# Performance work log

Hardware: AMD Instinct MI355X
Metric: run time of the kernel (lower is better)

Reference implementation:

```python
import jax, jax.numpy as jnp
import numpy as np

B, T, D, N, K, H = 2, 2048, 2560, 8, 4, 256
G = N // K
WINDOW = 1024
ROPE_BASE = 10000
K_MASK = -2.3819763e+38
EPS = 1e-6


def apply_rope(inputs, positions, base_frequency):
    # inputs: [B, L, n, H]; positions: [B, L]
    head_dim = inputs.shape[-1]
    fraction = 2 * jnp.arange(0, head_dim // 2) / head_dim
    timescale = base_frequency ** fraction
    sinusoid = positions[..., None] / timescale[None, None, :]   # [B, L, H/2]
    sinusoid = sinusoid[..., None, :]                            # [B, L, 1, H/2]
    sin, cos = jnp.sin(sinusoid), jnp.cos(sinusoid)
    first, second = jnp.split(inputs, 2, axis=-1)
    out = jnp.concatenate([first * cos - second * sin,
                           second * cos + first * sin], axis=-1)
    return out.astype(inputs.dtype)


def rms_norm(x, scale):
    # Gemma-style RMSNorm: normalize over last dim, (1 + scale) gain.
    var = jnp.mean(jnp.square(x), axis=-1, keepdims=True)
    return x * jax.lax.rsqrt(var + EPS) * (1.0 + scale)


def setup_inputs() -> dict:
    key = jax.random.key(0)
    ks = jax.random.split(key, 5)
    x = jax.random.normal(ks[0], (B, T, D), jnp.float32)
    positions = jnp.broadcast_to(jnp.arange(T, dtype=jnp.int32), (B, T))
    # Causal sliding-window mask (LOCAL_SLIDING, window=1024), shape [B, 1, T, S].
    qp = jnp.arange(T)[:, None]
    kp = jnp.arange(T)[None, :]
    mask = (kp <= qp) & ((qp - kp) < WINDOW)
    attn_mask = jnp.broadcast_to(mask[None, None], (B, 1, T, T))
    q_w = jax.random.normal(ks[1], (N, D, H), jnp.float32) * 0.02
    kv_w = jax.random.normal(ks[2], (2, K, D, H), jnp.float32) * 0.02
    q_scale = jnp.zeros((H,), jnp.float32)
    k_scale = jnp.zeros((H,), jnp.float32)
    out_w = jax.random.normal(ks[3], (N, H, D), jnp.float32) * 0.02
    return {"x": x, "q_w": q_w, "kv_w": kv_w, "q_scale": q_scale,
            "k_scale": k_scale, "out_w": out_w,
            "positions": positions, "attn_mask": attn_mask}


def reference(x, q_w, kv_w, q_scale, k_scale, out_w, positions, attn_mask):
    dtype = x.dtype
    # GQA projections (num_kv_heads != num_heads branch)
    q = jnp.einsum('BTD,NDH->BTNH', x, q_w)          # [B,T,N,H]
    k = jnp.einsum('BSD,KDH->BSKH', x, kv_w[0])      # [B,S,K,H]
    v = jnp.einsum('BSD,KDH->BSKH', x, kv_w[1])      # [B,S,K,H]
    # QK-RMSNorm (GQA branch only)
    q = rms_norm(q, q_scale)
    k = rms_norm(k, k_scale)
    # RoPE + query scaling
    q = apply_rope(q, positions, ROPE_BASE)
    q = q * (H ** -0.5)
    k = apply_rope(k, positions, ROPE_BASE)
    # Grouped attention logits: [B,T,K,G,S] -> [B,T,N,S]
    qg = q.reshape(B, T, K, G, H)
    logits = jnp.einsum('BTKGH,BSKH->BTKGS', qg, k)
    logits = logits.reshape(B, T, N, T)
    # Mask + softmax (mask [B,1,T,S] -> [B,T,1,S])
    bmask = jnp.expand_dims(attn_mask.squeeze(axis=1), axis=2)
    masked = jnp.where(bmask, logits, K_MASK)
    probs = jax.nn.softmax(masked, axis=-1).astype(dtype)
    # Weighted values with grouped kv heads
    pg = probs.reshape(B, T, K, G, T)
    enc = jnp.einsum('BTKGS,BSKH->BTKGH', pg, v).reshape(B, T, N, H)
    out = jnp.einsum('BTNH,NHD->BTD', enc, out_w)
    return out
```

## Files before the change

### kernel.cpp

```cpp
#include <hip/hip_runtime.h>
#include <cstdint>

#define TB 2048
#define DIM 2560
#define NQ 8
#define NKV 4
#define HDIM 256
#define WIN 1024
#define KMASK -2.3819763e+38f

using f32x4 = __attribute__((ext_vector_type(4))) float;
using s16x8 = __attribute__((ext_vector_type(8))) short;
using u16x4 = __attribute__((ext_vector_type(4))) unsigned short;

__device__ __forceinline__ unsigned short f2bf(float f) {
  uint32_t x = __builtin_bit_cast(uint32_t, f);
  x += 0x7FFFu + ((x >> 16) & 1u);
  return (unsigned short)(x >> 16);
}

__global__ __launch_bounds__(256) void k_packw1(const float* __restrict__ q_w,
                                                const float* __restrict__ kv_w,
                                                unsigned short* __restrict__ W1) {
  __shared__ float tile[32][33];
  const int hd = blockIdx.z;
  const float* src = (hd < 8) ? (q_w + (size_t)hd * DIM * HDIM)
                              : (kv_w + (size_t)(hd - 8) * DIM * HDIM);
  unsigned short* dst = W1 + (size_t)hd * HDIM * DIM;
  const int c0 = blockIdx.x * 32, r0 = blockIdx.y * 32;
  const int tx = threadIdx.x & 31, ty = threadIdx.x >> 5;
#pragma unroll
  for (int i = 0; i < 32; i += 8)
    tile[ty + i][tx] = src[(size_t)(r0 + ty + i) * HDIM + c0 + tx];
  __syncthreads();
#pragma unroll
  for (int i = 0; i < 32; i += 8)
    dst[(size_t)(c0 + ty + i) * DIM + r0 + tx] = f2bf(tile[tx][ty + i]);
}

__global__ __launch_bounds__(256) void k_tconv(const float* __restrict__ src,
                                               unsigned short* __restrict__ dst,
                                               int R, int C) {
  __shared__ float tile[32][33];
  const int c0 = blockIdx.x * 32, r0 = blockIdx.y * 32;
  const int tx = threadIdx.x & 31, ty = threadIdx.x >> 5;
#pragma unroll
  for (int i = 0; i < 32; i += 8)
    tile[ty + i][tx] = src[(size_t)(r0 + ty + i) * C + c0 + tx];
  __syncthreads();
#pragma unroll
  for (int i = 0; i < 32; i += 8)
    dst[(size_t)(c0 + ty + i) * R + r0 + tx] = f2bf(tile[tx][ty + i]);
}

__global__ __launch_bounds__(256) void k_cvt(const float* __restrict__ src,
                                             unsigned short* __restrict__ dst, int n4) {
  int i = blockIdx.x * 256 + threadIdx.x;
  if (i < n4) {
    f32x4 v = *(const f32x4*)&src[(size_t)i * 4];
    u16x4 o;
#pragma unroll
    for (int j = 0; j < 4; ++j) o[j] = f2bf(v[j]);
    *(u16x4*)&dst[(size_t)i * 4] = o;
  }
}

__global__ __launch_bounds__(512, 2) void k_gemm(const unsigned short* __restrict__ A,
                                                 const unsigned short* __restrict__ Bw,
                                                 float* __restrict__ Cc,
                                                 int Nc, int Kd, int nxl) {
  __shared__ unsigned short shA[2][256 * 64];
  __shared__ unsigned short shB[2][256 * 64];
  const int tid = threadIdx.x, w = tid >> 6, l = tid & 63;
  const int xcd = blockIdx.x & 7, loc = blockIdx.x >> 3;
  const int m0 = ((xcd >> 1) * 4 + loc / nxl) * 256;
  const int n0 = ((xcd & 1) * nxl + loc % nxl) * 256;

  const int srow = l >> 3;
  const int sw_colb = (((l & 7) ^ srow) << 4);
  const int wrow = w * 8;
  const int NT = Kd >> 6;

#define GSTAGE(buf, t)                                                                      \
  {                                                                                         \
    const size_t kt = (size_t)(t) << 6;                                                     \
    _Pragma("unroll") for (int r = 0; r < 4; ++r) {                                         \
      const char* src = (const char*)A + ((size_t)(m0 + r * 64 + wrow + srow) * Kd + kt) * 2 + sw_colb; \
      __builtin_amdgcn_global_load_lds(                                                     \
          (__attribute__((address_space(1))) void*)src,                                     \
          (__attribute__((address_space(3))) void*)((char*)&shA[buf][0] + r * 8192 + w * 1024), \
          16, 0, 0);                                                                        \
    }                                                                                       \
    _Pragma("unroll") for (int r = 0; r < 4; ++r) {                                         \
      const char* src = (const char*)Bw + ((size_t)(n0 + r * 64 + wrow + srow) * Kd + kt) * 2 + sw_colb; \
      __builtin_amdgcn_global_load_lds(                                                     \
          (__attribute__((address_space(1))) void*)src,                                     \
          (__attribute__((address_space(3))) void*)((char*)&shB[buf][0] + r * 8192 + w * 1024), \
          16, 0, 0);                                                                        \
    }                                                                                       \
  }

  const int wm = w >> 2, wn = w & 3;
  const int lr = l & 15, lg = l >> 4;
  f32x4 acc[8][4] = {};

  GSTAGE(0, 0);

  for (int t = 0; t < NT; ++t) {
    const int buf = t & 1;
    if (t + 1 < NT) {
      GSTAGE(buf ^ 1, t + 1);
      asm volatile("s_waitcnt vmcnt(8)" ::: "memory");
    } else {
      asm volatile("s_waitcnt vmcnt(0)" ::: "memory");
    }
    __builtin_amdgcn_s_barrier();

    const char* sa = (const char*)&shA[buf][0];
    const char* sb = (const char*)&shB[buf][0];
#pragma unroll
    for (int kk = 0; kk < 2; ++kk) {
      const int cb = kk * 64 + lg * 16;
      const int cbx = cb ^ ((lr & 7) << 4);
      s16x8 af[8], bfr[4];
#pragma unroll
      for (int mi = 0; mi < 8; ++mi)
        af[mi] = *(const s16x8*)(sa + (wm * 128 + mi * 16 + lr) * 128 + cbx);
#pragma unroll
      for (int ni = 0; ni < 4; ++ni)
        bfr[ni] = *(const s16x8*)(sb + (wn * 64 + ni * 16 + lr) * 128 + cbx);
      __builtin_amdgcn_s_setprio(1);
#pragma unroll
      for (int mi = 0; mi < 8; ++mi)
#pragma unroll
        for (int ni = 0; ni < 4; ++ni)
          acc[mi][ni] = __builtin_amdgcn_mfma_f32_16x16x32_bf16(af[mi], bfr[ni], acc[mi][ni], 0, 0, 0);
      __builtin_amdgcn_s_setprio(0);
    }
    __builtin_amdgcn_s_barrier();
  }
#undef GSTAGE

#pragma unroll
  for (int mi = 0; mi < 8; ++mi)
#pragma unroll
    for (int ni = 0; ni < 4; ++ni) {
      size_t base = (size_t)(m0 + wm * 128 + mi * 16 + lg * 4) * Nc + (n0 + wn * 64 + ni * 16 + lr);
#pragma unroll
      for (int i = 0; i < 4; ++i)
        Cc[base + (size_t)i * Nc] = acc[mi][ni][i];
    }
}

__global__ __launch_bounds__(256) void k_normrope(const float* __restrict__ Y,
                                                  const float* __restrict__ qsc,
                                                  const float* __restrict__ ksc,
                                                  const int* __restrict__ pos,
                                                  unsigned short* __restrict__ Q,
                                                  unsigned short* __restrict__ Kb) {
  __shared__ float s_sin[128], s_cos[128];
  const int bt = blockIdx.x;
  const int b = bt >> 11, t = bt & (TB - 1);
  const int tid = threadIdx.x;
  float p = (float)pos[bt];
  if (tid < 128) {
    float fr = (float)tid * (1.0f / 128.0f);
    float inv_ts = __expf(fr * -9.210340371976184f);
    float ang = p * inv_ts;
    float sv, cv;
    sincosf(ang, &sv, &cv);
    s_sin[tid] = sv;
    s_cos[tid] = cv;
  }
  __syncthreads();
  const int w = tid >> 6, l = tid & 63;
  const int jj0 = (l & 31) * 4;
  for (int sidx = w; sidx < 12; sidx += 4) {
    const float* src = Y + (size_t)bt * 4096 + sidx * 256;
    f32x4 v = *(const f32x4*)&src[l * 4];
    float ss = v[0] * v[0] + v[1] * v[1] + v[2] * v[2] + v[3] * v[3];
#pragma unroll
    for (int d = 1; d < 64; d <<= 1) ss += __shfl_xor(ss, d);
    float rs = rsqrtf(ss * (1.0f / 256.0f) + 1e-6f);
    const float* scp = (sidx < 8) ? qsc : ksc;
    float nv[4], res[4];
#pragma unroll
    for (int j = 0; j < 4; ++j) nv[j] = v[j] * rs * (1.0f + scp[l * 4 + j]);
#pragma unroll
    for (int j = 0; j < 4; ++j) {
      float o = __shfl_xor(nv[j], 32);
      float sn = s_sin[jj0 + j], cs = s_cos[jj0 + j];
      res[j] = (l < 32) ? (nv[j] * cs - o * sn) : (nv[j] * cs + o * sn);
    }
    float qs = (sidx < 8) ? 0.0625f : 1.0f;
    u16x4 ob;
#pragma unroll
    for (int j = 0; j < 4; ++j) ob[j] = f2bf(res[j] * qs);
    if (sidx < 8) {
      size_t di = ((size_t)(b * NQ + sidx) * TB + t) * HDIM + l * 4;
      *(u16x4*)&Q[di] = ob;
    } else {
      size_t di = ((size_t)(b * NKV + (sidx - 8)) * TB + t) * HDIM + l * 4;
      *(u16x4*)&Kb[di] = ob;
    }
  }
}

__global__ __launch_bounds__(256) void k_vtrans(const float* __restrict__ Y,
                                                unsigned short* __restrict__ VT) {
  __shared__ float tile[64][65];
  const int t0 = blockIdx.x * 64, h0 = blockIdx.y * 64;
  const int z = blockIdx.z;
  const int bq = z >> 2, kh = z & 3;
  const int tid = threadIdx.x;
#pragma unroll
  for (int rep = 0; rep < 16; ++rep) {
    int idx = rep * 256 + tid;
    int tr = idx >> 6, hc = idx & 63;
    tile[tr][hc] = Y[(size_t)(bq * TB + t0 + tr) * 4096 + 3072 + kh * 256 + h0 + hc];
  }
  __syncthreads();
#pragma unroll
  for (int rep = 0; rep < 16; ++rep) {
    int idx = rep * 256 + tid;
    int hr = idx >> 6, tc = idx & 63;
    VT[((size_t)z * 256 + h0 + hr) * TB + t0 + tc] = f2bf(tile[tc][hr]);
  }
}

__global__ __launch_bounds__(256, 2) void k_attn(const unsigned short* __restrict__ Q,
                                                 const unsigned short* __restrict__ Kb,
                                                 const unsigned short* __restrict__ VT,
                                                 unsigned short* __restrict__ ENC) {
  __shared__ unsigned short shK[2][32 * 256];
  __shared__ unsigned short shV[2][256 * 32];
  __shared__ unsigned short Pb[4][512];
  const int tid = threadIdx.x, w = tid >> 6, l = tid & 63;
  const int bn = blockIdx.y;
  const int b = bn >> 3, n = bn & 7, kh = n >> 1;
  const int t0b = blockIdx.x * 64;
  const int t0 = t0b + w * 16;
  const int lr = l & 15, lg = l >> 4;
  const unsigned short* qp = Q + ((size_t)bn * TB + t0) * HDIM;
  const char* kbase = (const char*)(Kb + ((size_t)(b * NKV + kh) * TB) * HDIM);
  const char* vbase = (const char*)(VT + ((size_t)(b * NKV + kh) * HDIM) * TB);

  s16x8 aq[8];
#pragma unroll
  for (int kk = 0; kk < 8; ++kk)
    aq[kk] = *(const s16x8*)&qp[lr * HDIM + kk * 32 + lg * 8];

  f32x4 o[16] = {};
  float mrow[4], lsum[4];
#pragma unroll
  for (int i = 0; i < 4; ++i) { mrow[i] = -__builtin_inff(); lsum[i] = 0.f; }

  int lo = t0b - (WIN - 1);
  if (lo < 0) lo = 0;
  lo &= ~31;
  const int nsteps = (t0b + 32 - lo) / 32 + 1;

  const int k_row = (w << 1) + (l >> 5);
  const int k_colb = (l & 31) * 16;
  const int v_row = (w << 4) + (l >> 2);
  const int v_colb = (l & 3) * 16;
#define STAGE(buf, s0)                                                                       \
  {                                                                                          \
    _Pragma("unroll") for (int r = 0; r < 4; ++r) {                                          \
      int row = r * 8 + k_row;                                                               \
      int scol = k_colb ^ ((row & 7) << 4);                                                  \
      const char* src = kbase + (size_t)((s0) + row) * 512 + scol;                           \
      __builtin_amdgcn_global_load_lds(                                                      \
          (__attribute__((address_space(1))) void*)src,                                      \
          (__attribute__((address_space(3))) void*)((char*)&shK[buf][0] + r * 4096 + w * 1024), \
          16, 0, 0);                                                                         \
    }                                                                                        \
    _Pragma("unroll") for (int r = 0; r < 4; ++r) {                                          \
      int row = r * 64 + v_row;                                                              \
      const char* src = vbase + (size_t)row * (TB * 2) + (size_t)(s0) * 2 + v_colb;          \
      __builtin_amdgcn_global_load_lds(                                                      \
          (__attribute__((address_space(1))) void*)src,                                      \
          (__attribute__((address_space(3))) void*)((char*)&shV[buf][0] + r * 4096 + w * 1024), \
          16, 0, 0);                                                                         \
    }                                                                                        \
  }

  STAGE(0, lo);
  __syncthreads();

  for (int step = 0; step < nsteps; ++step) {
    const int s0 = lo + step * 32;
    const int buf = step & 1;
    if (step + 1 < nsteps) STAGE(buf ^ 1, s0 + 32);

    const bool active = (s0 <= t0 + 15) && (s0 + 31 >= t0 - (WIN - 1));
    if (active) {
      f32x4 sacc[2] = {};
      const char* kt = (const char*)&shK[buf][0];
      const int swz = (lr & 7) << 4;
#pragma unroll
      for (int cb = 0; cb < 2; ++cb) {
        const int rb = (cb * 16 + lr) * 512;
#pragma unroll
        for (int kk = 0; kk < 8; ++kk) {
          s16x8 bk = *(const s16x8*)(kt + rb + ((kk * 64 + lg * 16) ^ swz));
          sacc[cb] = __builtin_amdgcn_mfma_f32_16x16x32_bf16(aq[kk], bk, sacc[cb], 0, 0, 0);
        }
      }
      float r_[4], p0[4], p1[4];
#pragma unroll
      for (int i = 0; i < 4; ++i) {
        int trow = t0 + lg * 4 + i;
        int sA = s0 + lr, sB = s0 + 16 + lr;
        float svA = ((sA <= trow) && (trow - sA < WIN)) ? sacc[0][i] : KMASK;
        float svB = ((sB <= trow) && (trow - sB < WIN)) ? sacc[1][i] : KMASK;
        float mx = fmaxf(svA, svB);
#pragma unroll
        for (int d = 1; d < 16; d <<= 1) mx = fmaxf(mx, __shfl_xor(mx, d));
        float mnew = fmaxf(mrow[i], mx);
        float r = __expf(mrow[i] - mnew);
        float pa = __expf(svA - mnew);
        float pb = __expf(svB - mnew);
        float bs = pa + pb;
#pragma unroll
        for (int d = 1; d < 16; d <<= 1) bs += __shfl_xor(bs, d);
        lsum[i] = lsum[i] * r + bs;
        mrow[i] = mnew;
        r_[i] = r; p0[i] = pa; p1[i] = pb;
      }
#pragma unroll
      for (int hb = 0; hb < 16; ++hb)
#pragma unroll
        for (int i = 0; i < 4; ++i) o[hb][i] *= r_[i];
#pragma unroll
      for (int i = 0; i < 4; ++i) {
        int row = lg * 4 + i;
        Pb[w][row * 32 + lr] = f2bf(p0[i]);
        Pb[w][row * 32 + 16 + lr] = f2bf(p1[i]);
      }
      asm volatile("s_waitcnt lgkmcnt(0)" ::: "memory");
      s16x8 pfrag = *(const s16x8*)&Pb[w][lr * 32 + lg * 8];
      const char* vt = (const char*)&shV[buf][0];
#pragma unroll
      for (int hb = 0; hb < 16; ++hb) {
        s16x8 vb = *(const s16x8*)(vt + (hb * 16 + lr) * 64 + lg * 16);
        o[hb] = __builtin_amdgcn_mfma_f32_16x16x32_bf16(pfrag, vb, o[hb], 0, 0, 0);
      }
    }
    __syncthreads();
  }
#undef STAGE

#pragma unroll
  for (int i = 0; i < 4; ++i) {
    int trow = t0 + lg * 4 + i;
    float inv = 1.0f / lsum[i];
    size_t rb = (size_t)(b * TB + trow) * 2048 + n * HDIM;
#pragma unroll
    for (int hb = 0; hb < 16; ++hb)
      ENC[rb + hb * 16 + lr] = f2bf(o[hb][i] * inv);
  }
}

extern "C" void kernel_launch(void* const* d_in, const int* in_sizes, int n_in,
                              void* d_out, int out_size, void* d_ws, size_t ws_size,
                              hipStream_t stream) {
  (void)in_sizes; (void)n_in; (void)out_size; (void)ws_size;
  const float* x = (const float*)d_in[0];
  const float* q_w = (const float*)d_in[1];
  const float* kv_w = (const float*)d_in[2];
  const float* qsc = (const float*)d_in[3];
  const float* ksc = (const float*)d_in[4];
  const float* out_w = (const float*)d_in[5];
  const int* pos = (const int*)d_in[6];
  float* out = (float*)d_out;

  char* ws = (char*)d_ws;
  unsigned short* W1 = (unsigned short*)(ws);
  unsigned short* W3 = (unsigned short*)(ws + 20971520);
  unsigned short* XB = (unsigned short*)(ws + 31457280);
  float* Y = (float*)(ws + 52428800);
  unsigned short* KB = (unsigned short*)(ws + 119537664);
  unsigned short* VT = (unsigned short*)(ws + 127926272);
  unsigned short* Qb = XB;
  unsigned short* ENC = (unsigned short*)(ws + 52428800);

  k_packw1<<<dim3(8, 80, 16), 256, 0, stream>>>(q_w, kv_w, W1);
  k_tconv<<<dim3(80, 64), 256, 0, stream>>>(out_w, W3, 2048, DIM);
  k_cvt<<<dim3(10240), 256, 0, stream>>>(x, XB, 2621440);
  k_gemm<<<dim3(256), 512, 0, stream>>>(XB, W1, Y, 4096, DIM, 8);
  k_normrope<<<dim3(4096), 256, 0, stream>>>(Y, qsc, ksc, pos, Qb, KB);
  k_vtrans<<<dim3(32, 4, 8), 256, 0, stream>>>(Y, VT);
  k_attn<<<dim3(32, 16), 256, 0, stream>>>(Qb, KB, VT, ENC);
  k_gemm<<<dim3(160), 512, 0, stream>>>(ENC, W3, out, DIM, 2048, 5);
}
```

Measured before the change: 297.4 us.

## Add lazy softmax rescale, mask skip, batched LDS loads and padded P buffer

The attention inner loop now skips the causal/window mask evaluation for tiles that lie entirely inside the valid band. It rescales the running max and output accumulator only when the new tile max exceeds the old by more than a threshold of 8, checked wave-wide. All K and V fragments are loaded from LDS before the MFMA chains, which are wrapped in s_setprio to favour matrix issue, and the P staging buffer is padded to 40 columns to reduce bank conflicts. The lazy rescale lets exponentials go above 1 (up to e^8), which narrows precision headroom in bf16 P values, and preloading V fragments raises register pressure under launch_bounds(256,2).

```diff
diff --git a/kernel.cpp b/kernel.cpp
--- a/kernel.cpp
+++ b/kernel.cpp
@@ -234,7 +234,7 @@
                                                  unsigned short* __restrict__ ENC) {
   __shared__ unsigned short shK[2][32 * 256];
   __shared__ unsigned short shV[2][256 * 32];
-  __shared__ unsigned short Pb[4][512];
+  __shared__ unsigned short Pb[4][16 * 40];
   const int tid = threadIdx.x, w = tid >> 6, l = tid & 63;
   const int bn = blockIdx.y;
   const int b = bn >> 3, n = bn & 7, kh = n >> 1;
@@ -301,51 +301,77 @@
 #pragma unroll
       for (int cb = 0; cb < 2; ++cb) {
         const int rb = (cb * 16 + lr) * 512;
-#pragma unroll
-        for (int kk = 0; kk < 8; ++kk) {
-          s16x8 bk = *(const s16x8*)(kt + rb + ((kk * 64 + lg * 16) ^ swz));
-          sacc[cb] = __builtin_amdgcn_mfma_f32_16x16x32_bf16(aq[kk], bk, sacc[cb], 0, 0, 0);
+        s16x8 bk[8];
+#pragma unroll
+        for (int kk = 0; kk < 8; ++kk)
+          bk[kk] = *(const s16x8*)(kt + rb + ((kk * 64 + lg * 16) ^ swz));
+        __builtin_amdgcn_s_setprio(1);
+#pragma unroll
+        for (int kk = 0; kk < 8; ++kk)
+          sacc[cb] = __builtin_amdgcn_mfma_f32_16x16x32_bf16(aq[kk], bk[kk], sacc[cb], 0, 0, 0);
+        __builtin_amdgcn_s_setprio(0);
+      }
+      float svA_[4], svB_[4], pmax[4];
+      const bool nomask = (s0 + 31 <= t0) && (s0 >= t0 - (WIN - 16));
+      if (nomask) {
+#pragma unroll
+        for (int i = 0; i < 4; ++i) { svA_[i] = sacc[0][i]; svB_[i] = sacc[1][i]; }
+      } else {
+#pragma unroll
+        for (int i = 0; i < 4; ++i) {
+          int trow = t0 + lg * 4 + i;
+          int sA = s0 + lr, sB = s0 + 16 + lr;
+          svA_[i] = ((sA <= trow) && (trow - sA < WIN)) ? sacc[0][i] : KMASK;
+          svB_[i] = ((sB <= trow) && (trow - sB < WIN)) ? sacc[1][i] : KMASK;
         }
       }
-      float r_[4], p0[4], p1[4];
 #pragma unroll
       for (int i = 0; i < 4; ++i) {
-        int trow = t0 + lg * 4 + i;
-        int sA = s0 + lr, sB = s0 + 16 + lr;
-        float svA = ((sA <= trow) && (trow - sA < WIN)) ? sacc[0][i] : KMASK;
-        float svB = ((sB <= trow) && (trow - sB < WIN)) ? sacc[1][i] : KMASK;
-        float mx = fmaxf(svA, svB);
+        float mx = fmaxf(svA_[i], svB_[i]);
 #pragma unroll
         for (int d = 1; d < 16; d <<= 1) mx = fmaxf(mx, __shfl_xor(mx, d));
-        float mnew = fmaxf(mrow[i], mx);
-        float r = __expf(mrow[i] - mnew);
-        float pa = __expf(svA - mnew);
-        float pb = __expf(svB - mnew);
+        pmax[i] = mx;
+      }
+      bool ok = (pmax[0] <= mrow[0] + 8.f) && (pmax[1] <= mrow[1] + 8.f) &&
+                (pmax[2] <= mrow[2] + 8.f) && (pmax[3] <= mrow[3] + 8.f);
+      if (!__all(ok)) {
+        float r_[4];
+#pragma unroll
+        for (int i = 0; i < 4; ++i) {
+          float mnew = fmaxf(mrow[i], pmax[i]);
+          r_[i] = __expf(mrow[i] - mnew);
+          lsum[i] *= r_[i];
+          mrow[i] = mnew;
+        }
+#pragma unroll
+        for (int hb = 0; hb < 16; ++hb)
+#pragma unroll
+          for (int i = 0; i < 4; ++i) o[hb][i] *= r_[i];
+      }
+#pragma unroll
+      for (int i = 0; i < 4; ++i) {
+        float pa = __expf(svA_[i] - mrow[i]);
+        float pb = __expf(svB_[i] - mrow[i]);
         float bs = pa + pb;
 #pragma unroll
         for (int d = 1; d < 16; d <<= 1) bs += __shfl_xor(bs, d);
-        lsum[i] = lsum[i] * r + bs;
-        mrow[i] = mnew;
-        r_[i] = r; p0[i] = pa; p1[i] = pb;
-      }
-#pragma unroll
-      for (int hb = 0; hb < 16; ++hb)
-#pragma unroll
-        for (int i = 0; i < 4; ++i) o[hb][i] *= r_[i];
-#pragma unroll
-      for (int i = 0; i < 4; ++i) {
+        lsum[i] += bs;
         int row = lg * 4 + i;
-        Pb[w][row * 32 + lr] = f2bf(p0[i]);
-        Pb[w][row * 32 + 16 + lr] = f2bf(p1[i]);
+        Pb[w][row * 40 + lr] = f2bf(pa);
+        Pb[w][row * 40 + 16 + lr] = f2bf(pb);
       }
       asm volatile("s_waitcnt lgkmcnt(0)" ::: "memory");
-      s16x8 pfrag = *(const s16x8*)&Pb[w][lr * 32 + lg * 8];
+      s16x8 pfrag = *(const s16x8*)&Pb[w][lr * 40 + lg * 8];
       const char* vt = (const char*)&shV[buf][0];
-#pragma unroll
-      for (int hb = 0; hb < 16; ++hb) {
-        s16x8 vb = *(const s16x8*)(vt + (hb * 16 + lr) * 64 + lg * 16);
-        o[hb] = __builtin_amdgcn_mfma_f32_16x16x32_bf16(pfrag, vb, o[hb], 0, 0, 0);
-      }
+      s16x8 vb[16];
+#pragma unroll
+      for (int hb = 0; hb < 16; ++hb)
+        vb[hb] = *(const s16x8*)(vt + (hb * 16 + lr) * 64 + lg * 16);
+      __builtin_amdgcn_s_setprio(1);
+#pragma unroll
+      for (int hb = 0; hb < 16; ++hb)
+        o[hb] = __builtin_amdgcn_mfma_f32_16x16x32_bf16(pfrag, vb[hb], o[hb], 0, 0, 0);
+      __builtin_amdgcn_s_setprio(0);
     }
     __syncthreads();
   }
```

Result: no change. 296.5 us (-0.3%).
